# Performance work log

Hardware: AMD Instinct MI355X
Metric: run time of the kernel (lower is better)

The kernel has to match this reference:

```python
import jax, jax.numpy as jnp
import numpy as np

B, S, D, H = 4, 2048, 1024, 16


def setup_inputs() -> dict:
    key = jax.random.key(0)
    ks = jax.random.split(key, 5)
    scale = 1.0 / np.sqrt(D)
    return {
        "q": jax.random.normal(ks[0], (B, S, D), jnp.float32),
        "v": jax.random.normal(ks[1], (B, S, D), jnp.float32),
        "Wq": jax.random.normal(ks[2], (D, D), jnp.float32) * scale,
        "bq": jnp.zeros((D,), jnp.float32),
        "Wk": jax.random.normal(ks[3], (D, D), jnp.float32) * scale,
        "bk": jnp.zeros((D,), jnp.float32),
        "Wv": jax.random.normal(ks[4], (D, D), jnp.float32) * scale,
        "bv": jnp.zeros((D,), jnp.float32),
    }


def reference(q, v, Wq, bq, Wk, bk, Wv, bv):
    # k defaults to v in the original call
    k = v
    embed_dim = Wq.shape[0]
    num_heads = H
    dh = embed_dim // num_heads
    b, s, _ = q.shape

    qp = q @ Wq + bq  # [B,S,D]
    kp = k @ Wk + bk
    vp = v @ Wv + bv

    # tf.split(x, H, axis=2) + concat on axis 0 == reshape to [B,S,H,dh]
    qh = qp.reshape(b, s, num_heads, dh)
    kh = kp.reshape(b, s, num_heads, dh)
    vh = vp.reshape(b, s, num_heads, dh)

    # NOTE: original scales by sqrt(embed_dim), NOT sqrt(head_dim)
    scores = jnp.einsum("bqhd,bkhd->bhqk", qh, kh) / jnp.sqrt(
        jnp.asarray(embed_dim, qh.dtype)
    )
    att = jax.nn.softmax(scores, axis=-1)
    out = jnp.einsum("bhqk,bkhd->bqhd", att, vh)
    return out.reshape(b, s, embed_dim)
```

## Files before the change

kernel.cpp:

```cpp
#include <hip/hip_runtime.h>
#include <hip/hip_bf16.h>
#include <math.h>

#define B_   4
#define S_   2048
#define D_   1024
#define H_   16
#define DH_  64
#define M_   (B_ * S_)
#define BH_  (B_ * H_)

typedef __bf16 bf16x8_t __attribute__((ext_vector_type(8)));
typedef float  f32x4_t  __attribute__((ext_vector_type(4)));
typedef float  f32x16_t __attribute__((ext_vector_type(16)));

#define QSCALE 0.045084220027780106f

__device__ __forceinline__ unsigned short f2bf(float x) {
  unsigned int u = __float_as_uint(x);
  u += 0x7fffu + ((u >> 16) & 1u);
  return (unsigned short)(u >> 16);
}

__device__ __forceinline__ unsigned int pk2t(float lo, float hi) {
  return __builtin_amdgcn_perm(__float_as_uint(hi), __float_as_uint(lo), 0x07060302u);
}

__device__ __forceinline__ void async16(const void* g, void* l) {
  __builtin_amdgcn_global_load_lds(
      (__attribute__((address_space(1))) unsigned int*)(void*)g,
      (__attribute__((address_space(3))) unsigned int*)l, 16, 0, 0);
}

__global__ __launch_bounds__(256) void cvt_f32_bf16(
    const float* __restrict__ q, const float* __restrict__ v,
    unsigned short* __restrict__ qb, unsigned short* __restrict__ vb) {
  const float* src = blockIdx.y ? v : q;
  unsigned short* dst = blockIdx.y ? vb : qb;
  size_t i = ((size_t)blockIdx.x * 256 + threadIdx.x) * 4;
  float4 a = *(const float4*)(src + i);
  ushort4 o;
  o.x = f2bf(a.x); o.y = f2bf(a.y); o.z = f2bf(a.z); o.w = f2bf(a.w);
  *(ushort4*)(dst + i) = o;
}

__global__ void wtrans(const float* __restrict__ Wq, const float* __restrict__ Wk,
                       const float* __restrict__ Wv,
                       unsigned short* __restrict__ Wqt, unsigned short* __restrict__ Wkt,
                       unsigned short* __restrict__ Wvt) {
  int z = blockIdx.z;
  const float* W = (z == 0) ? Wq : (z == 1 ? Wk : Wv);
  unsigned short* Wt = (z == 0) ? Wqt : (z == 1 ? Wkt : Wvt);
  __shared__ float tile[32][33];
  int tx = threadIdx.x, ty = threadIdx.y;
  int n = blockIdx.x * 32 + tx;
#pragma unroll
  for (int i = 0; i < 4; ++i) {
    int k = blockIdx.y * 32 + ty + i * 8;
    tile[ty + i * 8][tx] = W[(size_t)k * D_ + n];
  }
  __syncthreads();
  int k2 = blockIdx.y * 32 + tx;
#pragma unroll
  for (int i = 0; i < 4; ++i) {
    int n2 = blockIdx.x * 32 + ty + i * 8;
    Wt[(size_t)n2 * D_ + k2] = f2bf(tile[tx][ty + i * 8]);
  }
}

__global__ __launch_bounds__(256) void proj_gemm(
    const unsigned short* __restrict__ Aq, const unsigned short* __restrict__ Av,
    const unsigned short* __restrict__ Wqt, const unsigned short* __restrict__ Wkt,
    const unsigned short* __restrict__ Wvt,
    const float* __restrict__ bq, const float* __restrict__ bk, const float* __restrict__ bv,
    unsigned short* __restrict__ qp, unsigned short* __restrict__ kp,
    unsigned short* __restrict__ vt) {
  int z = blockIdx.y;
  const unsigned short* A  = (z == 0) ? Aq : Av;
  const unsigned short* Wt = (z == 0) ? Wqt : (z == 1 ? Wkt : Wvt);
  const float* bias        = (z == 0) ? bq : (z == 1 ? bk : bv);
  unsigned short* outp     = (z == 0) ? qp : (z == 1 ? kp : vt);
  const float cs           = (z == 0) ? QSCALE : 1.0f;

  int lin = blockIdx.x;
  int xcd = lin & 7, j = lin >> 3;
  int m0 = (xcd * 8 + (j & 7)) * 128;
  int n0 = (j >> 3) * 128;

  __shared__ __attribute__((aligned(16))) unsigned short Alds[128 * 32];
  __shared__ __attribute__((aligned(16))) unsigned short Blds[128 * 32];

  int t = threadIdx.x;
  int lane = t & 63, wave = t >> 6;
  int lrow = lane & 15, lq = lane >> 4;
  int wm = (wave & 1) * 64, wn = (wave >> 1) * 64;

  f32x4_t acc[4][4];
#pragma unroll
  for (int i = 0; i < 4; ++i)
#pragma unroll
    for (int j2 = 0; j2 < 4; ++j2) acc[i][j2] = (f32x4_t){0.f, 0.f, 0.f, 0.f};

  for (int k0 = 0; k0 < D_; k0 += 32) {
    __syncthreads();
#pragma unroll
    for (int r = 0; r < 2; ++r) {
      int off = t * 16 + r * 4096;
      int row = off >> 6, slot = (off >> 4) & 3;
      int ch = (slot ^ (row >> 1)) & 3;
      async16((const char*)A  + ((size_t)(m0 + row) * D_ + k0) * 2 + ch * 16, (char*)Alds + off);
      async16((const char*)Wt + ((size_t)(n0 + row) * D_ + k0) * 2 + ch * 16, (char*)Blds + off);
    }
    __syncthreads();

    bf16x8_t af[4], bfr[4];
#pragma unroll
    for (int i = 0; i < 4; ++i) {
      int ra = wm + i * 16 + lrow;
      int rb = wn + i * 16 + lrow;
      af[i]  = *(const bf16x8_t*)(Alds + ra * 32 + ((lq ^ (ra >> 1)) & 3) * 8);
      bfr[i] = *(const bf16x8_t*)(Blds + rb * 32 + ((lq ^ (rb >> 1)) & 3) * 8);
    }
#pragma unroll
    for (int i = 0; i < 4; ++i)
#pragma unroll
      for (int j2 = 0; j2 < 4; ++j2)
        acc[i][j2] = __builtin_amdgcn_mfma_f32_16x16x32_bf16(af[i], bfr[j2], acc[i][j2], 0, 0, 0);
  }

#pragma unroll
  for (int j2 = 0; j2 < 4; ++j2) {
    int n = n0 + wn + j2 * 16 + lrow;
    float bv_ = bias[n];
    int h = n >> 6, d = n & 63;
#pragma unroll
    for (int i = 0; i < 4; ++i) {
      int mbase = m0 + wm + i * 16 + lq * 4;
      int b = mbase >> 11, s = mbase & 2047;
      if (z != 2) {
#pragma unroll
        for (int r = 0; r < 4; ++r)
          outp[(((size_t)(b * H_ + h) * S_ + (s + r)) << 6) + d] = f2bf((acc[i][j2][r] + bv_) * cs);
      } else {
        ushort4 pk;
        pk.x = f2bf(acc[i][j2][0] + bv_);
        pk.y = f2bf(acc[i][j2][1] + bv_);
        pk.z = f2bf(acc[i][j2][2] + bv_);
        pk.w = f2bf(acc[i][j2][3] + bv_);
        *(ushort4*)(outp + (((size_t)(b * H_ + h) * 64 + d) << 11) + s) = pk;
      }
    }
  }
}

__global__ __launch_bounds__(256, 2) void attn(
    const unsigned short* __restrict__ qp, const unsigned short* __restrict__ kp,
    const unsigned short* __restrict__ vt, float* __restrict__ out) {
  const int bh = blockIdx.x;
  const int qt = blockIdx.y;
  const int t = threadIdx.x;
  const int lane = t & 63, wave = t >> 6;
  const int h = lane >> 5, ln = lane & 31;

  __shared__ __attribute__((aligned(16))) unsigned short Klds[2][64 * 64];
  __shared__ __attribute__((aligned(16))) unsigned short Vlds[2][64 * 64];

  const int q0 = qt * 256 + wave * 64;

  bf16x8_t qf[2][4];
#pragma unroll
  for (int rt = 0; rt < 2; ++rt)
#pragma unroll
    for (int ks = 0; ks < 4; ++ks)
      qf[rt][ks] = *(const bf16x8_t*)(qp + ((size_t)bh * S_ + q0 + rt * 32 + ln) * 64 + ks * 16 + h * 8);

  f32x16_t o[2][2];
  float l[2] = {0.f, 0.f};
#pragma unroll
  for (int rt = 0; rt < 2; ++rt)
#pragma unroll
    for (int dt = 0; dt < 2; ++dt)
#pragma unroll
      for (int r = 0; r < 16; ++r) o[rt][dt][r] = 0.f;

  f32x16_t z16;
#pragma unroll
  for (int r = 0; r < 16; ++r) z16[r] = 0.f;

  const unsigned short* kg = kp + (size_t)bh * S_ * 64;
  const unsigned short* vg = vt + (size_t)bh * 64 * S_;

  auto stage = [&](int kb, int bi) {
#pragma unroll
    for (int r = 0; r < 2; ++r) {
      int off = t * 16 + r * 4096;
      int row = off >> 7, slot = (off >> 4) & 7;
      int ch = slot ^ (row & 7);
      async16((const char*)(kg + (size_t)(kb + row) * 64 + ch * 8), (char*)&Klds[bi][0] + off);
      async16((const char*)(vg + (size_t)row * S_ + kb + ch * 8), (char*)&Vlds[bi][0] + off);
    }
  };

  stage(0, 0);

  const int NT = S_ / 64;
  for (int it = 0; it < NT; ++it) {
    const int bi = it & 1;
    __syncthreads();
    if (it + 1 < NT) stage((it + 1) * 64, bi ^ 1);

    const unsigned short* Kb = &Klds[bi][0];
    const unsigned short* Vb = &Vlds[bi][0];

    f32x16_t st[2][2];
#pragma unroll
    for (int kt = 0; kt < 2; ++kt) {
      {
        int row = kt * 32 + ln;
        bf16x8_t kf = *(const bf16x8_t*)(Kb + row * 64 + (((0 + h) ^ (row & 7)) * 8));
        st[0][kt] = __builtin_amdgcn_mfma_f32_32x32x16_bf16(kf, qf[0][0], z16, 0, 0, 0);
        st[1][kt] = __builtin_amdgcn_mfma_f32_32x32x16_bf16(kf, qf[1][0], z16, 0, 0, 0);
      }
#pragma unroll
      for (int ks = 1; ks < 4; ++ks) {
        int row = kt * 32 + ln;
        bf16x8_t kf = *(const bf16x8_t*)(Kb + row * 64 + (((ks * 2 + h) ^ (row & 7)) * 8));
        st[0][kt] = __builtin_amdgcn_mfma_f32_32x32x16_bf16(kf, qf[0][ks], st[0][kt], 0, 0, 0);
        st[1][kt] = __builtin_amdgcn_mfma_f32_32x32x16_bf16(kf, qf[1][ks], st[1][kt], 0, 0, 0);
      }
    }

    unsigned int pkv[2][2][8];
#pragma unroll
    for (int rt = 0; rt < 2; ++rt) {
      float lp = 0.f;
#pragma unroll
      for (int kt = 0; kt < 2; ++kt)
#pragma unroll
        for (int i = 0; i < 8; ++i) {
          float p0 = __builtin_amdgcn_exp2f(st[rt][kt][2 * i]);
          float p1 = __builtin_amdgcn_exp2f(st[rt][kt][2 * i + 1]);
          lp += p0 + p1;
          pkv[rt][kt][i] = pk2t(p0, p1);
        }
      l[rt] += lp + __shfl_xor(lp, 32);
    }

    bf16x8_t pf[2][4];
#pragma unroll
    for (int rt = 0; rt < 2; ++rt)
#pragma unroll
      for (int ks = 0; ks < 4; ++ks) {
        int kt = ks >> 1, b = 4 * (ks & 1);
        unsigned int e0 = __shfl_xor(h ? pkv[rt][kt][b]     : pkv[rt][kt][b + 2], 32);
        unsigned int e1 = __shfl_xor(h ? pkv[rt][kt][b + 1] : pkv[rt][kt][b + 3], 32);
        union { unsigned int u[4]; bf16x8_t v; } fr;
        fr.u[0] = h ? e0 : pkv[rt][kt][b];
        fr.u[1] = h ? e1 : pkv[rt][kt][b + 1];
        fr.u[2] = h ? pkv[rt][kt][b + 2] : e0;
        fr.u[3] = h ? pkv[rt][kt][b + 3] : e1;
        pf[rt][ks] = fr.v;
      }

#pragma unroll
    for (int dt = 0; dt < 2; ++dt)
#pragma unroll
      for (int ks = 0; ks < 4; ++ks) {
        int row = dt * 32 + ln;
        bf16x8_t vf = *(const bf16x8_t*)(Vb + row * 64 + (((ks * 2 + h) ^ (row & 7)) * 8));
#pragma unroll
        for (int rt = 0; rt < 2; ++rt)
          o[rt][dt] = __builtin_amdgcn_mfma_f32_32x32x16_bf16(pf[rt][ks], vf, o[rt][dt], 0, 0, 0);
      }
  }

  const int b = bh >> 4, head = bh & 15;
#pragma unroll
  for (int rt = 0; rt < 2; ++rt)
#pragma unroll
    for (int r = 0; r < 16; ++r) {
      int rowl = (r & 3) + 8 * (r >> 2) + 4 * h;
      float li = __shfl(l[rt], rowl, 64);
      float inv = __builtin_amdgcn_rcpf(li);
      int rg = q0 + rt * 32 + rowl;
      float* op = out + ((size_t)b * S_ + rg) * D_ + head * 64 + ln;
      op[0]  = o[rt][0][r] * inv;
      op[32] = o[rt][1][r] * inv;
    }
}

extern "C" void kernel_launch(void* const* d_in, const int* in_sizes, int n_in,
                              void* d_out, int out_size, void* d_ws, size_t ws_size,
                              hipStream_t stream) {
  const float* q  = (const float*)d_in[0];
  const float* v  = (const float*)d_in[1];
  const float* Wq = (const float*)d_in[2];
  const float* bq = (const float*)d_in[3];
  const float* Wk = (const float*)d_in[4];
  const float* bk = (const float*)d_in[5];
  const float* Wv = (const float*)d_in[6];
  const float* bv = (const float*)d_in[7];
  float* out = (float*)d_out;

  char* ws = (char*)d_ws;
  unsigned short* qb  = (unsigned short*)(ws);
  unsigned short* vb  = (unsigned short*)(ws + (16u << 20));
  unsigned short* Wqt = (unsigned short*)(ws + (32u << 20));
  unsigned short* Wkt = (unsigned short*)(ws + (34u << 20));
  unsigned short* Wvt = (unsigned short*)(ws + (36u << 20));
  unsigned short* qpp = (unsigned short*)(ws + (38u << 20));
  unsigned short* kpp = (unsigned short*)(ws + (54u << 20));
  unsigned short* vtp = (unsigned short*)(ws + (70u << 20));

  hipLaunchKernelGGL(cvt_f32_bf16, dim3((M_ * D_) / 1024, 2), dim3(256), 0, stream,
                     q, v, qb, vb);
  hipLaunchKernelGGL(wtrans, dim3(32, 32, 3), dim3(32, 8), 0, stream,
                     Wq, Wk, Wv, Wqt, Wkt, Wvt);
  hipLaunchKernelGGL(proj_gemm, dim3(512, 3), dim3(256), 0, stream,
                     qb, vb, Wqt, Wkt, Wvt, bq, bk, bv, qpp, kpp, vtp);
  hipLaunchKernelGGL(attn, dim3(BH_, S_ / 256), dim3(256), 0, stream,
                     qpp, kpp, vtp, out);
}
```

Before: 274.3 us.

## Split attention keys across wave pairs and deepen projection GEMM K-tile

The attention kernel now gives each block 128 queries instead of 256. Two wave pairs each process half of every 64-key tile, then their partial outputs and row sums are reduced through shared memory before the store. This doubles the grid, halves per-wave accumulator work and raises the launch-bounds occupancy hint to 3 blocks. Separately, the projection GEMM stages 64-wide K slices with a new XOR swizzle, halving the number of barriers per tile. The trade-offs are a shared-memory reduction epilogue and loading K/V tiles twice as often overall.

```diff
diff --git a/kernel.cpp b/kernel.cpp
--- a/kernel.cpp
+++ b/kernel.cpp
@@ -87,8 +87,8 @@
   int m0 = (xcd * 8 + (j & 7)) * 128;
   int n0 = (j >> 3) * 128;
 
-  __shared__ __attribute__((aligned(16))) unsigned short Alds[128 * 32];
-  __shared__ __attribute__((aligned(16))) unsigned short Blds[128 * 32];
+  __shared__ __attribute__((aligned(16))) unsigned short Alds[128 * 64];
+  __shared__ __attribute__((aligned(16))) unsigned short Blds[128 * 64];
 
   int t = threadIdx.x;
   int lane = t & 63, wave = t >> 6;
@@ -101,31 +101,34 @@
 #pragma unroll
     for (int j2 = 0; j2 < 4; ++j2) acc[i][j2] = (f32x4_t){0.f, 0.f, 0.f, 0.f};
 
-  for (int k0 = 0; k0 < D_; k0 += 32) {
-    __syncthreads();
-#pragma unroll
-    for (int r = 0; r < 2; ++r) {
+  for (int k0 = 0; k0 < D_; k0 += 64) {
+    __syncthreads();
+#pragma unroll
+    for (int r = 0; r < 4; ++r) {
       int off = t * 16 + r * 4096;
-      int row = off >> 6, slot = (off >> 4) & 3;
-      int ch = (slot ^ (row >> 1)) & 3;
+      int row = off >> 7, slot = (off >> 4) & 7;
+      int ch = slot ^ (row & 7);
       async16((const char*)A  + ((size_t)(m0 + row) * D_ + k0) * 2 + ch * 16, (char*)Alds + off);
       async16((const char*)Wt + ((size_t)(n0 + row) * D_ + k0) * 2 + ch * 16, (char*)Blds + off);
     }
     __syncthreads();
 
-    bf16x8_t af[4], bfr[4];
-#pragma unroll
-    for (int i = 0; i < 4; ++i) {
-      int ra = wm + i * 16 + lrow;
-      int rb = wn + i * 16 + lrow;
-      af[i]  = *(const bf16x8_t*)(Alds + ra * 32 + ((lq ^ (ra >> 1)) & 3) * 8);
-      bfr[i] = *(const bf16x8_t*)(Blds + rb * 32 + ((lq ^ (rb >> 1)) & 3) * 8);
-    }
-#pragma unroll
-    for (int i = 0; i < 4; ++i)
-#pragma unroll
-      for (int j2 = 0; j2 < 4; ++j2)
-        acc[i][j2] = __builtin_amdgcn_mfma_f32_16x16x32_bf16(af[i], bfr[j2], acc[i][j2], 0, 0, 0);
+#pragma unroll
+    for (int kk = 0; kk < 2; ++kk) {
+      bf16x8_t af[4], bfr[4];
+#pragma unroll
+      for (int i = 0; i < 4; ++i) {
+        int ra = wm + i * 16 + lrow;
+        int rb = wn + i * 16 + lrow;
+        af[i]  = *(const bf16x8_t*)((const char*)Alds + ra * 128 + (((lq + 4 * kk) ^ (ra & 7)) * 16));
+        bfr[i] = *(const bf16x8_t*)((const char*)Blds + rb * 128 + (((lq + 4 * kk) ^ (rb & 7)) * 16));
+      }
+#pragma unroll
+      for (int i = 0; i < 4; ++i)
+#pragma unroll
+        for (int j2 = 0; j2 < 4; ++j2)
+          acc[i][j2] = __builtin_amdgcn_mfma_f32_16x16x32_bf16(af[i], bfr[j2], acc[i][j2], 0, 0, 0);
+    }
   }
 
 #pragma unroll
@@ -153,7 +156,7 @@
   }
 }
 
-__global__ __launch_bounds__(256, 2) void attn(
+__global__ __launch_bounds__(256, 3) void attn(
     const unsigned short* __restrict__ qp, const unsigned short* __restrict__ kp,
     const unsigned short* __restrict__ vt, float* __restrict__ out) {
   const int bh = blockIdx.x;
@@ -161,11 +164,13 @@
   const int t = threadIdx.x;
   const int lane = t & 63, wave = t >> 6;
   const int h = lane >> 5, ln = lane & 31;
+  const int rhalf = wave & 1;
+  const int pairsel = wave >> 1;
 
   __shared__ __attribute__((aligned(16))) unsigned short Klds[2][64 * 64];
   __shared__ __attribute__((aligned(16))) unsigned short Vlds[2][64 * 64];
 
-  const int q0 = qt * 256 + wave * 64;
+  const int q0 = qt * 128 + rhalf * 64;
 
   bf16x8_t qf[2][4];
 #pragma unroll
@@ -204,6 +209,7 @@
   stage(0, 0);
 
   const int NT = S_ / 64;
+  const int krow = pairsel * 32 + ln;
   for (int it = 0; it < NT; ++it) {
     const int bi = it & 1;
     __syncthreads();
@@ -212,81 +218,110 @@
     const unsigned short* Kb = &Klds[bi][0];
     const unsigned short* Vb = &Vlds[bi][0];
 
-    f32x16_t st[2][2];
-#pragma unroll
-    for (int kt = 0; kt < 2; ++kt) {
-      {
-        int row = kt * 32 + ln;
-        bf16x8_t kf = *(const bf16x8_t*)(Kb + row * 64 + (((0 + h) ^ (row & 7)) * 8));
-        st[0][kt] = __builtin_amdgcn_mfma_f32_32x32x16_bf16(kf, qf[0][0], z16, 0, 0, 0);
-        st[1][kt] = __builtin_amdgcn_mfma_f32_32x32x16_bf16(kf, qf[1][0], z16, 0, 0, 0);
-      }
-#pragma unroll
-      for (int ks = 1; ks < 4; ++ks) {
-        int row = kt * 32 + ln;
-        bf16x8_t kf = *(const bf16x8_t*)(Kb + row * 64 + (((ks * 2 + h) ^ (row & 7)) * 8));
-        st[0][kt] = __builtin_amdgcn_mfma_f32_32x32x16_bf16(kf, qf[0][ks], st[0][kt], 0, 0, 0);
-        st[1][kt] = __builtin_amdgcn_mfma_f32_32x32x16_bf16(kf, qf[1][ks], st[1][kt], 0, 0, 0);
-      }
-    }
-
-    unsigned int pkv[2][2][8];
+    f32x16_t st[2];
+    {
+      bf16x8_t kf = *(const bf16x8_t*)(Kb + krow * 64 + ((h ^ (krow & 7)) * 8));
+      st[0] = __builtin_amdgcn_mfma_f32_32x32x16_bf16(kf, qf[0][0], z16, 0, 0, 0);
+      st[1] = __builtin_amdgcn_mfma_f32_32x32x16_bf16(kf, qf[1][0], z16, 0, 0, 0);
+    }
+#pragma unroll
+    for (int ks = 1; ks < 4; ++ks) {
+      bf16x8_t kf = *(const bf16x8_t*)(Kb + krow * 64 + (((ks * 2 + h) ^ (krow & 7)) * 8));
+      st[0] = __builtin_amdgcn_mfma_f32_32x32x16_bf16(kf, qf[0][ks], st[0], 0, 0, 0);
+      st[1] = __builtin_amdgcn_mfma_f32_32x32x16_bf16(kf, qf[1][ks], st[1], 0, 0, 0);
+    }
+
+    unsigned int pkv[2][8];
 #pragma unroll
     for (int rt = 0; rt < 2; ++rt) {
       float lp = 0.f;
 #pragma unroll
-      for (int kt = 0; kt < 2; ++kt)
-#pragma unroll
-        for (int i = 0; i < 8; ++i) {
-          float p0 = __builtin_amdgcn_exp2f(st[rt][kt][2 * i]);
-          float p1 = __builtin_amdgcn_exp2f(st[rt][kt][2 * i + 1]);
-          lp += p0 + p1;
-          pkv[rt][kt][i] = pk2t(p0, p1);
-        }
-      l[rt] += lp + __shfl_xor(lp, 32);
-    }
-
-    bf16x8_t pf[2][4];
+      for (int i = 0; i < 8; ++i) {
+        float p0 = __builtin_amdgcn_exp2f(st[rt][2 * i]);
+        float p1 = __builtin_amdgcn_exp2f(st[rt][2 * i + 1]);
+        lp += p0 + p1;
+        pkv[rt][i] = pk2t(p0, p1);
+      }
+      l[rt] += lp;
+    }
+
+    bf16x8_t pf[2][2];
 #pragma unroll
     for (int rt = 0; rt < 2; ++rt)
 #pragma unroll
-      for (int ks = 0; ks < 4; ++ks) {
-        int kt = ks >> 1, b = 4 * (ks & 1);
-        unsigned int e0 = __shfl_xor(h ? pkv[rt][kt][b]     : pkv[rt][kt][b + 2], 32);
-        unsigned int e1 = __shfl_xor(h ? pkv[rt][kt][b + 1] : pkv[rt][kt][b + 3], 32);
+      for (int ks2 = 0; ks2 < 2; ++ks2) {
+        int b = 4 * ks2;
+        unsigned int e0 = __shfl_xor(h ? pkv[rt][b]     : pkv[rt][b + 2], 32);
+        unsigned int e1 = __shfl_xor(h ? pkv[rt][b + 1] : pkv[rt][b + 3], 32);
         union { unsigned int u[4]; bf16x8_t v; } fr;
-        fr.u[0] = h ? e0 : pkv[rt][kt][b];
-        fr.u[1] = h ? e1 : pkv[rt][kt][b + 1];
-        fr.u[2] = h ? pkv[rt][kt][b + 2] : e0;
-        fr.u[3] = h ? pkv[rt][kt][b + 3] : e1;
-        pf[rt][ks] = fr.v;
-      }
-
-#pragma unroll
-    for (int dt = 0; dt < 2; ++dt)
-#pragma unroll
-      for (int ks = 0; ks < 4; ++ks) {
-        int row = dt * 32 + ln;
-        bf16x8_t vf = *(const bf16x8_t*)(Vb + row * 64 + (((ks * 2 + h) ^ (row & 7)) * 8));
+        fr.u[0] = h ? e0 : pkv[rt][b];
+        fr.u[1] = h ? e1 : pkv[rt][b + 1];
+        fr.u[2] = h ? pkv[rt][b + 2] : e0;
+        fr.u[3] = h ? pkv[rt][b + 3] : e1;
+        pf[rt][ks2] = fr.v;
+      }
+
+#pragma unroll
+    for (int dt = 0; dt < 2; ++dt) {
+      int vrow = dt * 32 + ln;
+#pragma unroll
+      for (int ks2 = 0; ks2 < 2; ++ks2) {
+        bf16x8_t vf = *(const bf16x8_t*)(Vb + vrow * 64 +
+                       (((pairsel * 4 + ks2 * 2 + h) ^ (vrow & 7)) * 8));
+        o[0][dt] = __builtin_amdgcn_mfma_f32_32x32x16_bf16(pf[0][ks2], vf, o[0][dt], 0, 0, 0);
+        o[1][dt] = __builtin_amdgcn_mfma_f32_32x32x16_bf16(pf[1][ks2], vf, o[1][dt], 0, 0, 0);
+      }
+    }
+  }
+
+#pragma unroll
+  for (int rt = 0; rt < 2; ++rt) l[rt] += __shfl_xor(l[rt], 32);
+
+  float* redo = (float*)&Klds[0][0];
+  float* redl = (float*)&Vlds[0][0];
+#pragma unroll
+  for (int dt = 0; dt < 2; ++dt) {
+    __syncthreads();
+    if (pairsel == 1) {
+#pragma unroll
+      for (int rt = 0; rt < 2; ++rt)
+#pragma unroll
+        for (int r = 0; r < 16; ++r)
+          redo[(((rhalf * 2) + rt) * 16 + r) * 64 + lane] = o[rt][dt][r];
+      if (dt == 0)
 #pragma unroll
         for (int rt = 0; rt < 2; ++rt)
-          o[rt][dt] = __builtin_amdgcn_mfma_f32_32x32x16_bf16(pf[rt][ks], vf, o[rt][dt], 0, 0, 0);
-      }
-  }
-
-  const int b = bh >> 4, head = bh & 15;
-#pragma unroll
-  for (int rt = 0; rt < 2; ++rt)
-#pragma unroll
-    for (int r = 0; r < 16; ++r) {
-      int rowl = (r & 3) + 8 * (r >> 2) + 4 * h;
-      float li = __shfl(l[rt], rowl, 64);
-      float inv = __builtin_amdgcn_rcpf(li);
-      int rg = q0 + rt * 32 + rowl;
-      float* op = out + ((size_t)b * S_ + rg) * D_ + head * 64 + ln;
-      op[0]  = o[rt][0][r] * inv;
-      op[32] = o[rt][1][r] * inv;
-    }
+          redl[((rhalf * 2) + rt) * 64 + lane] = l[rt];
+    }
+    __syncthreads();
+    if (pairsel == 0) {
+#pragma unroll
+      for (int rt = 0; rt < 2; ++rt)
+#pragma unroll
+        for (int r = 0; r < 16; ++r)
+          o[rt][dt][r] += redo[(((rhalf * 2) + rt) * 16 + r) * 64 + lane];
+      if (dt == 0)
+#pragma unroll
+        for (int rt = 0; rt < 2; ++rt)
+          l[rt] += redl[((rhalf * 2) + rt) * 64 + lane];
+    }
+  }
+
+  if (pairsel == 0) {
+    const int b = bh >> 4, head = bh & 15;
+#pragma unroll
+    for (int rt = 0; rt < 2; ++rt)
+#pragma unroll
+      for (int r = 0; r < 16; ++r) {
+        int rowl = (r & 3) + 8 * (r >> 2) + 4 * h;
+        float li = __shfl(l[rt], rowl, 64);
+        float inv = __builtin_amdgcn_rcpf(li);
+        int rg = q0 + rt * 32 + rowl;
+        float* op = out + ((size_t)b * S_ + rg) * D_ + head * 64 + ln;
+        op[0]  = o[rt][0][r] * inv;
+        op[32] = o[rt][1][r] * inv;
+      }
+  }
 }
 
 extern "C" void kernel_launch(void* const* d_in, const int* in_sizes, int n_in,
@@ -318,6 +353,6 @@
                      Wq, Wk, Wv, Wqt, Wkt, Wvt);
   hipLaunchKernelGGL(proj_gemm, dim3(512, 3), dim3(256), 0, stream,
                      qb, vb, Wqt, Wkt, Wvt, bq, bk, bv, qpp, kpp, vtp);
-  hipLaunchKernelGGL(attn, dim3(BH_, S_ / 256), dim3(256), 0, stream,
+  hipLaunchKernelGGL(attn, dim3(BH_, S_ / 128), dim3(256), 0, stream,
                      qpp, kpp, vtp, out);
 }
```

Result: slower. 289.0 us (+5.4%).
